# Performance work log

Measured on AMD Instinct MI355X. Metric: run time of the kernel, lower is better.

Reference implementation:

```python
import jax, jax.numpy as jnp
import numpy as np

B, BS, M, D = 64, 8, 512, 256  # b = bs * neg_sample_num, neg_sample_num = 8
NEG_FILL = -1e10


def setup_inputs() -> dict:
    key = jax.random.key(0)
    ks = jax.random.split(key, 7)
    x = jax.random.normal(ks[0], (B, M, D), jnp.float32)
    y = jax.random.normal(ks[1], (BS, M, D), jnp.float32)
    mask_x = jax.random.randint(ks[2], (B, M), 0, 2).astype(bool).at[:, 0].set(True)
    mask_y = jax.random.randint(ks[3], (BS, M), 0, 2).astype(bool).at[:, 0].set(True)
    scale = 1.0 / np.sqrt(D)
    Wq = jax.random.normal(ks[4], (D, D), jnp.float32) * scale  # torch Linear weight [out,in]
    Wk = jax.random.normal(ks[5], (D, D), jnp.float32) * scale
    Wv = jax.random.normal(ks[6], (D, D), jnp.float32) * scale
    return {"x": x, "y": y, "mask_x": mask_x, "mask_y": mask_y, "Wq": Wq, "Wk": Wk, "Wv": Wv}


def reference(x, y, mask_x, mask_y, Wq, Wk, Wv):
    # Projections (torch Linear: x @ W.T, no bias)
    Qx, Kx, Vx = x @ Wq.T, x @ Wk.T, x @ Wv.T
    Qy, Ky, Vy = y @ Wq.T, y @ Wk.T, y @ Wv.T
    b, m, d = Qx.shape
    bs = Ky.shape[0]
    neg = b // bs  # neg_sample_num branch (bs != b)

    scores_x = jnp.einsum('bid,bjd->bij', Qx, Kx)   # [b,m,m]
    scores_y = jnp.einsum('bid,bjd->bij', Qy, Ky)   # [bs,m,m]
    # Q_x grouped as [bs, neg, m, d] then transposed to [neg, bs, m, d];
    # K_y is tiled over neg (pure broadcast), so contract directly against [bs,m,d].
    Qx_e = Qx.reshape(bs, neg, m, d).swapaxes(0, 1)  # [neg,bs,m,d]
    scores_xy = jnp.einsum('nsid,sjd->nsij', Qx_e, Ky)  # [neg,bs,m,m]

    mx = mask_x[:, :, None]  # [b,m,1]
    my = mask_y[:, :, None]  # [bs,m,1]
    scores_x = jnp.where(mx & mx.swapaxes(1, 2), scores_x, NEG_FILL)
    scores_y = jnp.where(my & my.swapaxes(1, 2), scores_y, NEG_FILL)

    mask_xy = mask_x.reshape(bs, neg, m, 1).swapaxes(0, 1) & mask_y[None, :, None, :]  # [neg,bs,m,m]
    scores_xy = jnp.where(mask_xy, scores_xy, NEG_FILL)

    # y_len[n, s] = sum(mask_y[s]) for every n (repeat/view/sum/transpose in torch)
    y_len = jnp.broadcast_to(jnp.sum(mask_y.astype(jnp.int32), axis=1)[None, :], (neg, bs))

    probs_x = jax.nn.softmax(scores_x, axis=-1)
    probs_y = jax.nn.softmax(scores_y, axis=-1)
    probs_xy = jax.nn.softmax(scores_xy, axis=-1)

    ctx_x = jnp.einsum('bij,bjd->bid', probs_x, Vx)
    ctx_y = jnp.einsum('bij,bjd->bid', probs_y, Vy)
    return (ctx_x, ctx_y, scores_x, scores_y, probs_xy, mask_xy, y_len)
```

## Files before the change

kernel.cpp:

```cpp
#include <hip/hip_runtime.h>
#include <cstdint>

#define NEG_FILL_F (-10000000000.0f)
constexpr int BB     = 64;
constexpr int BS_    = 8;
constexpr int MM     = 512;
constexpr int DD     = 256;
constexpr int ROWS_X = BB * MM;
constexpr int ROWS_Y = BS_ * MM;
constexpr int ROWS_ALL = ROWS_X + ROWS_Y;
constexpr int K3     = 768;

typedef __attribute__((ext_vector_type(8))) short short8;
typedef __attribute__((ext_vector_type(4))) float f32x4;

__device__ inline unsigned short rne_bf16(float f) {
    unsigned int u = __float_as_uint(f);
    u = (u + 0x7FFFu + ((u >> 16) & 1u)) >> 16;
    return (unsigned short)u;
}
__device__ inline float bf2f(unsigned short h) {
    return __uint_as_float(((unsigned int)h) << 16);
}

__device__ inline f32x4 mfma16(short8 a, short8 b, f32x4 c) {
    return __builtin_amdgcn_mfma_f32_16x16x32_bf16(a, b, c, 0, 0, 0);
}

__device__ inline void gld16(const unsigned short* g, unsigned short* l) {
    __builtin_amdgcn_global_load_lds(
        (const __attribute__((address_space(1))) unsigned int*)g,
        (__attribute__((address_space(3))) unsigned int*)l, 16, 0, 0);
}

template<int LDA, int LDB>
__device__ inline void mfma_tiles(const unsigned short (*Ab)[LDA],
                                  const unsigned short (*Bb)[LDB],
                                  int kk, int wrow, int wcol, int lid, int quad,
                                  f32x4 acc[4][4])
{
    short8 af[4], bfr[4];
    #pragma unroll
    for (int i = 0; i < 4; ++i)
        af[i] = *(const short8*)&Ab[wrow + i * 16 + lid][kk + quad * 8];
    #pragma unroll
    for (int j = 0; j < 4; ++j)
        bfr[j] = *(const short8*)&Bb[wcol + j * 16 + lid][kk + quad * 8];
    #pragma unroll
    for (int i = 0; i < 4; ++i)
        #pragma unroll
        for (int j = 0; j < 4; ++j)
            acc[i][j] = mfma16(af[i], bfr[j], acc[i][j]);
}

__device__ inline void stage768_async(unsigned short* dstbase,
                                      const unsigned short* __restrict__ src,
                                      int ck, int wave, int lane)
{
    #pragma unroll
    for (int s = 0; s < 6; ++s) {
        const int c   = s * 256 + wave * 64 + lane;
        const int row = c / 12;
        const int kc  = (c % 12) * 8;
        gld16(src + (size_t)row * K3 + ck * 96 + kc,
              dstbase + (size_t)(s * 256 + wave * 64) * 8);
    }
}

__device__ inline void stage_x96(unsigned short (*dst)[96],
                                 const float* __restrict__ src,
                                 int ck, int t)
{
    #pragma unroll
    for (int s = 0; s < 4; ++s) {
        const int c   = s * 256 + t;
        const int row = c >> 3;
        const int q4  = (c & 7) * 4;
        float4 v = *(const float4*)(src + (size_t)row * DD + ck * 32 + q4);
        const float fv[4] = {v.x, v.y, v.z, v.w};
        unsigned short o[12];
        #pragma unroll
        for (int e = 0; e < 4; ++e) {
            unsigned short h = rne_bf16(fv[e]);
            unsigned short l = rne_bf16(fv[e] - bf2f(h));
            o[e*3+0] = h; o[e*3+1] = l; o[e*3+2] = h;
        }
        ushort4* p = (ushort4*)&dst[row][q4 * 3];
        p[0] = make_ushort4(o[0], o[1], o[2],  o[3]);
        p[1] = make_ushort4(o[4], o[5], o[6],  o[7]);
        p[2] = make_ushort4(o[8], o[9], o[10], o[11]);
    }
}

__global__ __launch_bounds__(256) void convw_kernel(
    const float* __restrict__ Wq, const float* __restrict__ Wk,
    const float* __restrict__ Wv, unsigned short* __restrict__ Wb)
{
    const int g  = blockIdx.x * 256 + threadIdx.x;
    const int e  = g * 8;
    const int zi = e >> 16;
    const int off = e & 65535;
    const float* W = (zi == 0) ? Wq : (zi == 1 ? Wk : Wv);
    float4 v0 = *(const float4*)(W + off);
    float4 v1 = *(const float4*)(W + off + 4);
    const float fv[8] = {v0.x, v0.y, v0.z, v0.w, v1.x, v1.y, v1.z, v1.w};
    unsigned short o[24];
    #pragma unroll
    for (int i = 0; i < 8; ++i) {
        unsigned short h = rne_bf16(fv[i]);
        unsigned short l = rne_bf16(fv[i] - bf2f(h));
        o[i*3+0] = h; o[i*3+1] = h; o[i*3+2] = l;
    }
    unsigned short* dst = Wb + (size_t)zi * 196608 + (size_t)off * 3;
    #pragma unroll
    for (int s = 0; s < 3; ++s) {
        short8 v;
        #pragma unroll
        for (int e2 = 0; e2 < 8; ++e2) v[e2] = (short)o[s*8+e2];
        *(short8*)(dst + s * 8) = v;
    }
}

__global__ __launch_bounds__(256) void proj_kernel(
    const float* __restrict__ x, const float* __restrict__ y,
    const unsigned short* __restrict__ Wb,
    unsigned short* __restrict__ Qa, unsigned short* __restrict__ Kb,
    unsigned short* __restrict__ Vt)
{
    const int z    = blockIdx.z;
    const int row0 = blockIdx.x * 128;
    const int col0 = blockIdx.y * 128;
    const float* A = (row0 < ROWS_X) ? (x + (size_t)row0 * DD)
                                     : (y + (size_t)(row0 - ROWS_X) * DD);
    const unsigned short* Bsrc = Wb + (size_t)z * 196608 + (size_t)col0 * K3;

    __shared__ unsigned short Ab[128][96];
    __shared__ unsigned short Bb[128][96];

    const int t = threadIdx.x;
    const int wave = t >> 6, lane = t & 63, quad = lane >> 4, lid = lane & 15;
    const int wrow = (wave & 1) * 64, wcol = (wave >> 1) * 64;

    f32x4 acc[4][4];
    #pragma unroll
    for (int i = 0; i < 4; ++i)
        #pragma unroll
        for (int j = 0; j < 4; ++j) acc[i][j] = (f32x4){0.f, 0.f, 0.f, 0.f};

    for (int ck = 0; ck < 8; ++ck) {
        stage768_async(&Bb[0][0], Bsrc, ck, wave, lane);
        stage_x96(Ab, A, ck, t);
        __syncthreads();
        #pragma unroll
        for (int kk = 0; kk < 96; kk += 32)
            mfma_tiles<96,96>(Ab, Bb, kk, wrow, wcol, lid, quad, acc);
        __syncthreads();
    }

    if (z == 2) {
        #pragma unroll
        for (int i = 0; i < 4; ++i) {
            const int rg = row0 + wrow + i * 16 + quad * 4;
            const int b  = rg >> 9;
            const int j  = rg & 511;
            #pragma unroll
            for (int jt = 0; jt < 4; ++jt) {
                const int col = col0 + wcol + jt * 16 + lid;
                *(ushort4*)(Vt + (size_t)b * DD * MM + (size_t)col * MM + j) =
                    make_ushort4(rne_bf16(acc[i][jt][0]), rne_bf16(acc[i][jt][1]),
                                 rne_bf16(acc[i][jt][2]), rne_bf16(acc[i][jt][3]));
            }
        }
    } else {
        unsigned short* dst = (z == 0) ? Qa : Kb;
        const bool aform = (z == 0);
        #pragma unroll
        for (int i = 0; i < 4; ++i) {
            const int rg = row0 + wrow + i * 16 + quad * 4;
            #pragma unroll
            for (int r = 0; r < 4; ++r) {
                unsigned short* rowp = dst + (size_t)(rg + r) * K3;
                #pragma unroll
                for (int jt = 0; jt < 4; ++jt) {
                    const int col = col0 + wcol + jt * 16 + lid;
                    const float v = acc[i][jt][r];
                    unsigned short h = rne_bf16(v);
                    unsigned short l = rne_bf16(v - bf2f(h));
                    rowp[3*col+0] = h;
                    rowp[3*col+1] = aform ? l : h;
                    rowp[3*col+2] = aform ? h : l;
                }
            }
        }
    }
}

__global__ __launch_bounds__(256) void scores_kernel(
    const unsigned short* __restrict__ Qa_base,
    const unsigned short* __restrict__ Kb_base,
    const int* __restrict__ mq_base, const int* __restrict__ mk_base,
    float* __restrict__ Sbase, float* __restrict__ Mbase,
    float2* __restrict__ pstats, int mode)
{
    const int z = blockIdx.z;
    int bq, bk;
    if (mode == 2) { const int n = z >> 3, s = z & 7; bq = s * 8 + n; bk = s; }
    else           { bq = z; bk = z; }

    const int row0 = blockIdx.x * 128;
    const int col0 = blockIdx.y * 128;
    const unsigned short* Asrc = Qa_base + (size_t)(bq * MM + row0) * K3;
    const unsigned short* Bsrc = Kb_base + (size_t)(bk * MM + col0) * K3;
    const int* mq = mq_base + bq * MM;
    const int* mk = mk_base + bk * MM;
    float* S  = Sbase + (size_t)z * MM * MM;
    float* Mo = (mode == 2) ? (Mbase + (size_t)z * MM * MM) : nullptr;

    __shared__ unsigned short Ab[128][96];
    __shared__ unsigned short Bb[128][96];
    __shared__ float pm2[128][2];
    __shared__ float ps2[128][2];

    const int t = threadIdx.x;
    const int wave = t >> 6, lane = t & 63, quad = lane >> 4, lid = lane & 15;
    const int wrow = (wave & 1) * 64, wcol = (wave >> 1) * 64;

    f32x4 acc[4][4];
    #pragma unroll
    for (int i = 0; i < 4; ++i)
        #pragma unroll
        for (int j = 0; j < 4; ++j) acc[i][j] = (f32x4){0.f, 0.f, 0.f, 0.f};

    for (int ck = 0; ck < 8; ++ck) {
        stage768_async(&Ab[0][0], Asrc, ck, wave, lane);
        stage768_async(&Bb[0][0], Bsrc, ck, wave, lane);
        __syncthreads();
        #pragma unroll
        for (int kk = 0; kk < 96; kk += 32)
            mfma_tiles<96,96>(Ab, Bb, kk, wrow, wcol, lid, quad, acc);
        __syncthreads();
    }

    int mcol[4];
    #pragma unroll
    for (int jt = 0; jt < 4; ++jt) mcol[jt] = mk[col0 + wcol + jt * 16 + lid];

    #pragma unroll
    for (int i = 0; i < 4; ++i) {
        const int rl0 = wrow + i * 16 + quad * 4;
        #pragma unroll
        for (int r = 0; r < 4; ++r) {
            const int rlocal = rl0 + r;
            const int rg = row0 + rlocal;
            const bool mr = (mq[rg] != 0);
            float* Srow = S + (size_t)rg * MM;
            float* Mrow = Mo ? (Mo + (size_t)rg * MM) : nullptr;
            float v[4];
            float mt = -3.4e38f;
            #pragma unroll
            for (int jt = 0; jt < 4; ++jt) {
                const int col = col0 + wcol + jt * 16 + lid;
                const bool valid = mr && (mcol[jt] != 0);
                v[jt] = valid ? acc[i][jt][r] : NEG_FILL_F;
                Srow[col] = v[jt];
                if (Mrow) Mrow[col] = valid ? 1.0f : 0.0f;
                mt = fmaxf(mt, v[jt]);
            }
            #pragma unroll
            for (int o = 1; o < 16; o <<= 1) mt = fmaxf(mt, __shfl_xor(mt, o));
            float se = 0.f;
            #pragma unroll
            for (int jt = 0; jt < 4; ++jt) se += __expf(v[jt] - mt);
            #pragma unroll
            for (int o = 1; o < 16; o <<= 1) se += __shfl_xor(se, o);
            if (lid == 0) { pm2[rlocal][wave >> 1] = mt; ps2[rlocal][wave >> 1] = se; }
        }
    }
    __syncthreads();
    if (t < 128) {
        const float m0 = pm2[t][0], m1 = pm2[t][1];
        const float mm = fmaxf(m0, m1);
        const float ss = ps2[t][0] * __expf(m0 - mm) + ps2[t][1] * __expf(m1 - mm);
        pstats[(size_t)(z * 4 + blockIdx.y) * MM + row0 + t] = make_float2(mm, ss);
    }
}

__global__ __launch_bounds__(256) void reduce4_kernel(
    const float2* __restrict__ p, float2* __restrict__ st)
{
    const int row = blockIdx.x * 256 + threadIdx.x;
    const int z = row >> 9, rl = row & 511;
    float m = -3.4e38f, s = 0.f;
    #pragma unroll
    for (int by = 0; by < 4; ++by) {
        float2 v = p[(size_t)(z * 4 + by) * MM + rl];
        float nm = fmaxf(m, v.x);
        s = s * __expf(m - nm) + v.y * __expf(v.x - nm);
        m = nm;
    }
    st[row] = make_float2(m, 1.0f / s);
}

__global__ __launch_bounds__(256) void ctx_kernel(
    const float* __restrict__ Sbase, const float2* __restrict__ stats,
    const unsigned short* __restrict__ Vt_base, float* __restrict__ Obase)
{
    const int b = blockIdx.z;
    const float*          S  = Sbase + (size_t)b * MM * MM;
    const float2*         st = stats + (size_t)b * MM;
    const unsigned short* Vt = Vt_base + (size_t)b * DD * MM;
    float*                O  = Obase + (size_t)b * MM * DD;

    const int row0 = blockIdx.x * 128;
    const int col0 = blockIdx.y * 128;

    __shared__ unsigned short Ab[128][72];
    __shared__ unsigned short Bb[128][64];

    const int t = threadIdx.x;
    const int wave = t >> 6, lane = t & 63, quad = lane >> 4, lid = lane & 15;
    const int wrow = (wave & 1) * 64, wcol = (wave >> 1) * 64;

    f32x4 acc[4][4];
    #pragma unroll
    for (int i = 0; i < 4; ++i)
        #pragma unroll
        for (int j = 0; j < 4; ++j) acc[i][j] = (f32x4){0.f, 0.f, 0.f, 0.f};

    for (int ck = 0; ck < 8; ++ck) {
        #pragma unroll
        for (int s = 0; s < 4; ++s) {
            const int c   = s * 256 + wave * 64 + lane;
            const int row = c >> 3;
            const int j8  = (c & 7) * 8;
            gld16(Vt + (size_t)(col0 + row) * MM + ck * 64 + j8,
                  &Bb[0][0] + (size_t)(s * 256 + wave * 64) * 8);
        }
        #pragma unroll
        for (int s = 0; s < 4; ++s) {
            const int c   = s * 256 + t;
            const int row = c >> 3;
            const int j8  = (c & 7) * 8;
            const float* sp = S + (size_t)(row0 + row) * MM + ck * 64 + j8;
            float4 v0 = *(const float4*)sp;
            float4 v1 = *(const float4*)(sp + 4);
            const float pm = st[row0 + row].x;
            short8 pk;
            pk[0] = (short)rne_bf16(__expf(v0.x - pm));
            pk[1] = (short)rne_bf16(__expf(v0.y - pm));
            pk[2] = (short)rne_bf16(__expf(v0.z - pm));
            pk[3] = (short)rne_bf16(__expf(v0.w - pm));
            pk[4] = (short)rne_bf16(__expf(v1.x - pm));
            pk[5] = (short)rne_bf16(__expf(v1.y - pm));
            pk[6] = (short)rne_bf16(__expf(v1.z - pm));
            pk[7] = (short)rne_bf16(__expf(v1.w - pm));
            *(short8*)&Ab[row][j8] = pk;
        }
        __syncthreads();
        #pragma unroll
        for (int kk = 0; kk < 64; kk += 32)
            mfma_tiles<72,64>(Ab, Bb, kk, wrow, wcol, lid, quad, acc);
        __syncthreads();
    }

    #pragma unroll
    for (int i = 0; i < 4; ++i) {
        const int rgb = row0 + wrow + i * 16 + quad * 4;
        float inv[4];
        #pragma unroll
        for (int r = 0; r < 4; ++r) inv[r] = st[rgb + r].y;
        #pragma unroll
        for (int jt = 0; jt < 4; ++jt) {
            const int col = col0 + wcol + jt * 16 + lid;
            #pragma unroll
            for (int r = 0; r < 4; ++r)
                O[(size_t)(rgb + r) * DD + col] = acc[i][jt][r] * inv[r];
        }
    }
}

__global__ __launch_bounds__(128) void softmax_apply(
    float* __restrict__ S, const float2* __restrict__ stats)
{
    const int row = blockIdx.x;
    const float2 st = stats[row];
    float4* r = (float4*)(S + (size_t)row * MM) + threadIdx.x;
    float4 v = *r;
    v.x = __expf(v.x - st.x) * st.y;
    v.y = __expf(v.y - st.x) * st.y;
    v.z = __expf(v.z - st.x) * st.y;
    v.w = __expf(v.w - st.x) * st.y;
    *r = v;
}

__global__ void ylen_kernel(const int* __restrict__ mask_y, float* __restrict__ out)
{
    const int s = blockIdx.x;
    const int lane = threadIdx.x;
    int c = 0;
    #pragma unroll
    for (int k = 0; k < 8; ++k) c += (mask_y[s * MM + k * 64 + lane] != 0);
    #pragma unroll
    for (int off = 32; off; off >>= 1) c += __shfl_xor(c, off);
    if (lane < 8) out[lane * 8 + s] = (float)c;
}

extern "C" void kernel_launch(void* const* d_in, const int* in_sizes, int n_in,
                              void* d_out, int out_size, void* d_ws, size_t ws_size,
                              hipStream_t stream)
{
    const float* x      = (const float*)d_in[0];
    const float* y      = (const float*)d_in[1];
    const int*   mask_x = (const int*)d_in[2];
    const int*   mask_y = (const int*)d_in[3];
    const float* Wq     = (const float*)d_in[4];
    const float* Wk     = (const float*)d_in[5];
    const float* Wv     = (const float*)d_in[6];
    float* out = (float*)d_out;

    unsigned short* Wb = (unsigned short*)d_ws;
    unsigned short* Qa = Wb + 589824;
    unsigned short* Kb = Qa + 28311552;
    unsigned short* Vt = Kb + 28311552;
    float2* stats_x  = (float2*)(Vt + 9437184);
    float2* stats_y  = stats_x + ROWS_X;
    float2* stats_xy = stats_y + ROWS_Y;
    float2* ps_x  = stats_xy + ROWS_X;
    float2* ps_y  = ps_x + 64 * 4 * 512;
    float2* ps_xy = ps_y + 8 * 4 * 512;

    float* out_ctx_x = out;
    float* out_ctx_y = out + 8388608;
    float* out_sx    = out + 9437184;
    float* out_sy    = out + 26214400;
    float* out_pxy   = out + 28311552;
    float* out_mxy   = out + 45088768;
    float* out_ylen  = out + 61865984;

    convw_kernel<<<96, 256, 0, stream>>>(Wq, Wk, Wv, Wb);

    proj_kernel<<<dim3(288, 2, 3), 256, 0, stream>>>(x, y, Wb, Qa, Kb, Vt);

    const unsigned short* Qa_y = Qa + (size_t)ROWS_X * K3;
    const unsigned short* Kb_y = Kb + (size_t)ROWS_X * K3;

    scores_kernel<<<dim3(4, 4, 64), 256, 0, stream>>>(Qa,   Kb,   mask_x, mask_x, out_sx,  nullptr, ps_x,  0);
    scores_kernel<<<dim3(4, 4, 8),  256, 0, stream>>>(Qa_y, Kb_y, mask_y, mask_y, out_sy,  nullptr, ps_y,  1);
    scores_kernel<<<dim3(4, 4, 64), 256, 0, stream>>>(Qa,   Kb_y, mask_x, mask_y, out_pxy, out_mxy, ps_xy, 2);

    reduce4_kernel<<<ROWS_X / 256, 256, 0, stream>>>(ps_x,  stats_x);
    reduce4_kernel<<<ROWS_Y / 256, 256, 0, stream>>>(ps_y,  stats_y);
    reduce4_kernel<<<ROWS_X / 256, 256, 0, stream>>>(ps_xy, stats_xy);

    ctx_kernel<<<dim3(4, 2, 64), 256, 0, stream>>>(out_sx, stats_x, Vt, out_ctx_x);
    ctx_kernel<<<dim3(4, 2, 8),  256, 0, stream>>>(out_sy, stats_y,
                                                   Vt + (size_t)64 * DD * MM, out_ctx_y);

    softmax_apply<<<ROWS_X, 128, 0, stream>>>(out_pxy, stats_xy);

    ylen_kernel<<<8, 64, 0, stream>>>(mask_y, out_ylen);
}
```

Baseline: 550.4 us.

## Split bf16x3 operands into separate hi/lo planes and stage epilogues via LDS

Replaces the interleaved 768-wide bf16x3 operand format with separate hi and lo bf16 arrays of width 256. A conversion kernel pre-splits x, y and the weights, so proj no longer converts activations inline. The GEMM loops become 12 chunks of 64 using the same three-product split. Proj epilogues now go through swizzled LDS for coalesced 16-byte stores, including the transposed V. The mask_xy output moves out of the scores kernel into its own kernel, and the ctx kernel hoists its row-max loads. This adds an extra pass over x/y and more barriers per GEMM, but cuts the byte-granular scattered stores.

```diff
diff --git a/kernel.cpp b/kernel.cpp
--- a/kernel.cpp
+++ b/kernel.cpp
@@ -9,7 +9,6 @@
 constexpr int ROWS_X = BB * MM;
 constexpr int ROWS_Y = BS_ * MM;
 constexpr int ROWS_ALL = ROWS_X + ROWS_Y;
-constexpr int K3     = 768;
 
 typedef __attribute__((ext_vector_type(8))) short short8;
 typedef __attribute__((ext_vector_type(4))) float f32x4;
@@ -22,11 +21,9 @@
 __device__ inline float bf2f(unsigned short h) {
     return __uint_as_float(((unsigned int)h) << 16);
 }
-
 __device__ inline f32x4 mfma16(short8 a, short8 b, f32x4 c) {
     return __builtin_amdgcn_mfma_f32_16x16x32_bf16(a, b, c, 0, 0, 0);
 }
-
 __device__ inline void gld16(const unsigned short* g, unsigned short* l) {
     __builtin_amdgcn_global_load_lds(
         (const __attribute__((address_space(1))) unsigned int*)g,
@@ -53,89 +50,68 @@
             acc[i][j] = mfma16(af[i], bfr[j], acc[i][j]);
 }
 
-__device__ inline void stage768_async(unsigned short* dstbase,
-                                      const unsigned short* __restrict__ src,
-                                      int ck, int wave, int lane)
-{
-    #pragma unroll
-    for (int s = 0; s < 6; ++s) {
+__device__ inline void stage64_async(unsigned short* dstbase,
+                                     const unsigned short* __restrict__ src,
+                                     int wave, int lane)
+{
+    #pragma unroll
+    for (int s = 0; s < 4; ++s) {
         const int c   = s * 256 + wave * 64 + lane;
-        const int row = c / 12;
-        const int kc  = (c % 12) * 8;
-        gld16(src + (size_t)row * K3 + ck * 96 + kc,
+        const int row = c >> 3;
+        const int off = (c & 7) * 8;
+        gld16(src + (size_t)row * 256 + off,
               dstbase + (size_t)(s * 256 + wave * 64) * 8);
     }
 }
 
-__device__ inline void stage_x96(unsigned short (*dst)[96],
-                                 const float* __restrict__ src,
-                                 int ck, int t)
-{
-    #pragma unroll
-    for (int s = 0; s < 4; ++s) {
-        const int c   = s * 256 + t;
-        const int row = c >> 3;
-        const int q4  = (c & 7) * 4;
-        float4 v = *(const float4*)(src + (size_t)row * DD + ck * 32 + q4);
-        const float fv[4] = {v.x, v.y, v.z, v.w};
-        unsigned short o[12];
-        #pragma unroll
-        for (int e = 0; e < 4; ++e) {
-            unsigned short h = rne_bf16(fv[e]);
-            unsigned short l = rne_bf16(fv[e] - bf2f(h));
-            o[e*3+0] = h; o[e*3+1] = l; o[e*3+2] = h;
-        }
-        ushort4* p = (ushort4*)&dst[row][q4 * 3];
-        p[0] = make_ushort4(o[0], o[1], o[2],  o[3]);
-        p[1] = make_ushort4(o[4], o[5], o[6],  o[7]);
-        p[2] = make_ushort4(o[8], o[9], o[10], o[11]);
-    }
-}
-
-__global__ __launch_bounds__(256) void convw_kernel(
+__global__ __launch_bounds__(256) void conv_kernel(
+    const float* __restrict__ x, const float* __restrict__ y,
     const float* __restrict__ Wq, const float* __restrict__ Wk,
-    const float* __restrict__ Wv, unsigned short* __restrict__ Wb)
-{
-    const int g  = blockIdx.x * 256 + threadIdx.x;
-    const int e  = g * 8;
-    const int zi = e >> 16;
-    const int off = e & 65535;
-    const float* W = (zi == 0) ? Wq : (zi == 1 ? Wk : Wv);
-    float4 v0 = *(const float4*)(W + off);
-    float4 v1 = *(const float4*)(W + off + 4);
+    const float* __restrict__ Wv,
+    unsigned short* __restrict__ Xh, unsigned short* __restrict__ Xl,
+    unsigned short* __restrict__ Wh, unsigned short* __restrict__ Wl)
+{
+    const size_t e = ((size_t)blockIdx.x * 256 + threadIdx.x) * 8;
+    const float* src; unsigned short *dh, *dl;
+    if (e < 9437184) {
+        src = (e < 8388608) ? (x + e) : (y + (e - 8388608));
+        dh = Xh + e; dl = Xl + e;
+    } else {
+        const size_t ew = e - 9437184;
+        const int zi = (int)(ew >> 16);
+        src = (zi == 0 ? Wq : zi == 1 ? Wk : Wv) + (ew & 65535);
+        dh = Wh + ew; dl = Wl + ew;
+    }
+    float4 v0 = *(const float4*)src;
+    float4 v1 = *(const float4*)(src + 4);
     const float fv[8] = {v0.x, v0.y, v0.z, v0.w, v1.x, v1.y, v1.z, v1.w};
-    unsigned short o[24];
+    short8 h8, l8;
     #pragma unroll
     for (int i = 0; i < 8; ++i) {
         unsigned short h = rne_bf16(fv[i]);
-        unsigned short l = rne_bf16(fv[i] - bf2f(h));
-        o[i*3+0] = h; o[i*3+1] = h; o[i*3+2] = l;
-    }
-    unsigned short* dst = Wb + (size_t)zi * 196608 + (size_t)off * 3;
-    #pragma unroll
-    for (int s = 0; s < 3; ++s) {
-        short8 v;
-        #pragma unroll
-        for (int e2 = 0; e2 < 8; ++e2) v[e2] = (short)o[s*8+e2];
-        *(short8*)(dst + s * 8) = v;
-    }
+        h8[i] = (short)h;
+        l8[i] = (short)rne_bf16(fv[i] - bf2f(h));
+    }
+    *(short8*)dh = h8;
+    *(short8*)dl = l8;
 }
 
 __global__ __launch_bounds__(256) void proj_kernel(
-    const float* __restrict__ x, const float* __restrict__ y,
-    const unsigned short* __restrict__ Wb,
-    unsigned short* __restrict__ Qa, unsigned short* __restrict__ Kb,
+    const unsigned short* __restrict__ Xh, const unsigned short* __restrict__ Xl,
+    const unsigned short* __restrict__ Wh, const unsigned short* __restrict__ Wl,
+    unsigned short* __restrict__ Qh, unsigned short* __restrict__ Ql,
+    unsigned short* __restrict__ Kh, unsigned short* __restrict__ Kl,
     unsigned short* __restrict__ Vt)
 {
     const int z    = blockIdx.z;
     const int row0 = blockIdx.x * 128;
     const int col0 = blockIdx.y * 128;
-    const float* A = (row0 < ROWS_X) ? (x + (size_t)row0 * DD)
-                                     : (y + (size_t)(row0 - ROWS_X) * DD);
-    const unsigned short* Bsrc = Wb + (size_t)z * 196608 + (size_t)col0 * K3;
-
-    __shared__ unsigned short Ab[128][96];
-    __shared__ unsigned short Bb[128][96];
+    const unsigned short* WhP = Wh + (size_t)z * 65536;
+    const unsigned short* WlP = Wl + (size_t)z * 65536;
+
+    __shared__ unsigned short POOL[16384];
+    unsigned short (*Ab)[64] = (unsigned short (*)[64])POOL;
+    unsigned short (*Bb)[64] = (unsigned short (*)[64])(POOL + 8192);
 
     const int t = threadIdx.x;
     const int wave = t >> 6, lane = t & 63, quad = lane >> 4, lid = lane & 15;
@@ -147,60 +123,86 @@
         #pragma unroll
         for (int j = 0; j < 4; ++j) acc[i][j] = (f32x4){0.f, 0.f, 0.f, 0.f};
 
-    for (int ck = 0; ck < 8; ++ck) {
-        stage768_async(&Bb[0][0], Bsrc, ck, wave, lane);
-        stage_x96(Ab, A, ck, t);
-        __syncthreads();
-        #pragma unroll
-        for (int kk = 0; kk < 96; kk += 32)
-            mfma_tiles<96,96>(Ab, Bb, kk, wrow, wcol, lid, quad, acc);
+    for (int ck = 0; ck < 12; ++ck) {
+        const int s  = ck >> 2;
+        const int d0 = (ck & 3) * 64;
+        const unsigned short* Ap = (s == 2 ? Xl : Xh) + (size_t)row0 * 256 + d0;
+        const unsigned short* Bp = (s == 1 ? WlP : WhP) + (size_t)col0 * 256 + d0;
+        stage64_async(&Ab[0][0], Ap, wave, lane);
+        stage64_async(&Bb[0][0], Bp, wave, lane);
+        __syncthreads();
+        mfma_tiles<64,64>(Ab, Bb, 0,  wrow, wcol, lid, quad, acc);
+        mfma_tiles<64,64>(Ab, Bb, 32, wrow, wcol, lid, quad, acc);
         __syncthreads();
     }
 
     if (z == 2) {
         #pragma unroll
         for (int i = 0; i < 4; ++i) {
-            const int rg = row0 + wrow + i * 16 + quad * 4;
-            const int b  = rg >> 9;
-            const int j  = rg & 511;
+            const int tok0 = wrow + i * 16 + quad * 4;
             #pragma unroll
             for (int jt = 0; jt < 4; ++jt) {
-                const int col = col0 + wcol + jt * 16 + lid;
-                *(ushort4*)(Vt + (size_t)b * DD * MM + (size_t)col * MM + j) =
-                    make_ushort4(rne_bf16(acc[i][jt][0]), rne_bf16(acc[i][jt][1]),
-                                 rne_bf16(acc[i][jt][2]), rne_bf16(acc[i][jt][3]));
+                const int d  = wcol + jt * 16 + lid;
+                const int sw = ((d >> 2) & 7) << 4;
+                unsigned int lo = (unsigned)rne_bf16(acc[i][jt][0]) |
+                                  ((unsigned)rne_bf16(acc[i][jt][1]) << 16);
+                unsigned int hi = (unsigned)rne_bf16(acc[i][jt][2]) |
+                                  ((unsigned)rne_bf16(acc[i][jt][3]) << 16);
+                *(uint2*)&POOL[d * 128 + (tok0 ^ sw)] = make_uint2(lo, hi);
             }
         }
+        __syncthreads();
+        const int dloc = t >> 1, cb = (t & 1) * 64;
+        const int sw = ((dloc >> 2) & 7) << 4;
+        const int b = row0 >> 9, j0 = row0 & 511;
+        unsigned short* gdst = Vt + ((size_t)b * DD + col0 + dloc) * MM + j0 + cb;
+        #pragma unroll
+        for (int g = 0; g < 8; ++g) {
+            short8 v = *(const short8*)&POOL[dloc * 128 + ((cb + g * 8) ^ sw)];
+            *(short8*)(gdst + g * 8) = v;
+        }
     } else {
-        unsigned short* dst = (z == 0) ? Qa : Kb;
-        const bool aform = (z == 0);
-        #pragma unroll
-        for (int i = 0; i < 4; ++i) {
-            const int rg = row0 + wrow + i * 16 + quad * 4;
-            #pragma unroll
-            for (int r = 0; r < 4; ++r) {
-                unsigned short* rowp = dst + (size_t)(rg + r) * K3;
+        unsigned short* dstH = (z == 0) ? Qh : Kh;
+        unsigned short* dstL = (z == 0) ? Ql : Kl;
+        #pragma unroll
+        for (int p = 0; p < 2; ++p) {
+            #pragma unroll
+            for (int i = 0; i < 4; ++i) {
+                const int rl = wrow + i * 16 + quad * 4;
                 #pragma unroll
-                for (int jt = 0; jt < 4; ++jt) {
-                    const int col = col0 + wcol + jt * 16 + lid;
-                    const float v = acc[i][jt][r];
-                    unsigned short h = rne_bf16(v);
-                    unsigned short l = rne_bf16(v - bf2f(h));
-                    rowp[3*col+0] = h;
-                    rowp[3*col+1] = aform ? l : h;
-                    rowp[3*col+2] = aform ? h : l;
+                for (int r = 0; r < 4; ++r) {
+                    const int row = rl + r;
+                    const int sw  = ((row >> 2) & 7) << 4;
+                    #pragma unroll
+                    for (int jt = 0; jt < 4; ++jt) {
+                        const int col = wcol + jt * 16 + lid;
+                        const float v = acc[i][jt][r];
+                        const unsigned short h = rne_bf16(v);
+                        POOL[row * 128 + (col ^ sw)] =
+                            (p == 0) ? h : rne_bf16(v - bf2f(h));
+                    }
                 }
             }
+            __syncthreads();
+            const int rr = t >> 1, cb = (t & 1) * 64;
+            const int sw = ((rr >> 2) & 7) << 4;
+            unsigned short* gdst = (p == 0 ? dstH : dstL)
+                                 + (size_t)(row0 + rr) * 256 + col0 + cb;
+            #pragma unroll
+            for (int g = 0; g < 8; ++g) {
+                short8 v = *(const short8*)&POOL[rr * 128 + ((cb + g * 8) ^ sw)];
+                *(short8*)(gdst + g * 8) = v;
+            }
+            __syncthreads();
         }
     }
 }
 
 __global__ __launch_bounds__(256) void scores_kernel(
-    const unsigned short* __restrict__ Qa_base,
-    const unsigned short* __restrict__ Kb_base,
+    const unsigned short* __restrict__ Qh_, const unsigned short* __restrict__ Ql_,
+    const unsigned short* __restrict__ Kh_, const unsigned short* __restrict__ Kl_,
     const int* __restrict__ mq_base, const int* __restrict__ mk_base,
-    float* __restrict__ Sbase, float* __restrict__ Mbase,
-    float2* __restrict__ pstats, int mode)
+    float* __restrict__ Sbase, float2* __restrict__ pstats, int mode)
 {
     const int z = blockIdx.z;
     int bq, bk;
@@ -209,15 +211,15 @@
 
     const int row0 = blockIdx.x * 128;
     const int col0 = blockIdx.y * 128;
-    const unsigned short* Asrc = Qa_base + (size_t)(bq * MM + row0) * K3;
-    const unsigned short* Bsrc = Kb_base + (size_t)(bk * MM + col0) * K3;
+    const size_t aoff = (size_t)(bq * MM + row0) * 256;
+    const size_t boff = (size_t)(bk * MM + col0) * 256;
     const int* mq = mq_base + bq * MM;
     const int* mk = mk_base + bk * MM;
-    float* S  = Sbase + (size_t)z * MM * MM;
-    float* Mo = (mode == 2) ? (Mbase + (size_t)z * MM * MM) : nullptr;
-
-    __shared__ unsigned short Ab[128][96];
-    __shared__ unsigned short Bb[128][96];
+    float* S = Sbase + (size_t)z * MM * MM;
+
+    __shared__ unsigned short POOL[16384];
+    unsigned short (*Ab)[64] = (unsigned short (*)[64])POOL;
+    unsigned short (*Bb)[64] = (unsigned short (*)[64])(POOL + 8192);
     __shared__ float pm2[128][2];
     __shared__ float ps2[128][2];
 
@@ -231,13 +233,16 @@
         #pragma unroll
         for (int j = 0; j < 4; ++j) acc[i][j] = (f32x4){0.f, 0.f, 0.f, 0.f};
 
-    for (int ck = 0; ck < 8; ++ck) {
-        stage768_async(&Ab[0][0], Asrc, ck, wave, lane);
-        stage768_async(&Bb[0][0], Bsrc, ck, wave, lane);
-        __syncthreads();
-        #pragma unroll
-        for (int kk = 0; kk < 96; kk += 32)
-            mfma_tiles<96,96>(Ab, Bb, kk, wrow, wcol, lid, quad, acc);
+    for (int ck = 0; ck < 12; ++ck) {
+        const int s  = ck >> 2;
+        const int d0 = (ck & 3) * 64;
+        const unsigned short* Ap = (s == 2 ? Ql_ : Qh_) + aoff + d0;
+        const unsigned short* Bp = (s == 1 ? Kl_ : Kh_) + boff + d0;
+        stage64_async(&Ab[0][0], Ap, wave, lane);
+        stage64_async(&Bb[0][0], Bp, wave, lane);
+        __syncthreads();
+        mfma_tiles<64,64>(Ab, Bb, 0,  wrow, wcol, lid, quad, acc);
+        mfma_tiles<64,64>(Ab, Bb, 32, wrow, wcol, lid, quad, acc);
         __syncthreads();
     }
 
@@ -254,7 +259,6 @@
             const int rg = row0 + rlocal;
             const bool mr = (mq[rg] != 0);
             float* Srow = S + (size_t)rg * MM;
-            float* Mrow = Mo ? (Mo + (size_t)rg * MM) : nullptr;
             float v[4];
             float mt = -3.4e38f;
             #pragma unroll
@@ -263,7 +267,6 @@
                 const bool valid = mr && (mcol[jt] != 0);
                 v[jt] = valid ? acc[i][jt][r] : NEG_FILL_F;
                 Srow[col] = v[jt];
-                if (Mrow) Mrow[col] = valid ? 1.0f : 0.0f;
                 mt = fmaxf(mt, v[jt]);
             }
             #pragma unroll
@@ -285,6 +288,28 @@
     }
 }
 
+__global__ __launch_bounds__(256) void maskxy_kernel(
+    const int* __restrict__ mask_x, const int* __restrict__ mask_y,
+    float* __restrict__ Mo)
+{
+    const int z = blockIdx.y;
+    const int n = z >> 3, s = z & 7, bq = s * 8 + n;
+    const int i = blockIdx.x * 4 + (threadIdx.x >> 6);
+    const int lane = threadIdx.x & 63;
+    const bool mr = mask_x[bq * MM + i] != 0;
+    float* row = Mo + ((size_t)z * MM + i) * MM;
+    const int4* my = (const int4*)(mask_y + s * MM);
+    #pragma unroll
+    for (int g = 0; g < 2; ++g) {
+        const int c4 = g * 64 + lane;
+        int4 m4 = my[c4];
+        float4 v = mr ? make_float4(m4.x ? 1.f : 0.f, m4.y ? 1.f : 0.f,
+                                    m4.z ? 1.f : 0.f, m4.w ? 1.f : 0.f)
+                      : make_float4(0.f, 0.f, 0.f, 0.f);
+        *(float4*)(row + c4 * 4) = v;
+    }
+}
+
 __global__ __launch_bounds__(256) void reduce4_kernel(
     const float2* __restrict__ p, float2* __restrict__ st)
 {
@@ -326,6 +351,10 @@
     for (int i = 0; i < 4; ++i)
         #pragma unroll
         for (int j = 0; j < 4; ++j) acc[i][j] = (f32x4){0.f, 0.f, 0.f, 0.f};
+
+    float pmv[4];
+    #pragma unroll
+    for (int s = 0; s < 4; ++s) pmv[s] = st[row0 + ((s * 256 + t) >> 3)].x;
 
     for (int ck = 0; ck < 8; ++ck) {
         #pragma unroll
@@ -344,7 +373,7 @@
             const float* sp = S + (size_t)(row0 + row) * MM + ck * 64 + j8;
             float4 v0 = *(const float4*)sp;
             float4 v1 = *(const float4*)(sp + 4);
-            const float pm = st[row0 + row].x;
+            const float pm = pmv[s];
             short8 pk;
             pk[0] = (short)rne_bf16(__expf(v0.x - pm));
             pk[1] = (short)rne_bf16(__expf(v0.y - pm));
@@ -357,9 +386,8 @@
             *(short8*)&Ab[row][j8] = pk;
         }
         __syncthreads();
-        #pragma unroll
-        for (int kk = 0; kk < 64; kk += 32)
-            mfma_tiles<72,64>(Ab, Bb, kk, wrow, wcol, lid, quad, acc);
+        mfma_tiles<72,64>(Ab, Bb, 0,  wrow, wcol, lid, quad, acc);
+        mfma_tiles<72,64>(Ab, Bb, 32, wrow, wcol, lid, quad, acc);
         __syncthreads();
     }
 
@@ -418,10 +446,15 @@
     const float* Wv     = (const float*)d_in[6];
     float* out = (float*)d_out;
 
-    unsigned short* Wb = (unsigned short*)d_ws;
-    unsigned short* Qa = Wb + 589824;
-    unsigned short* Kb = Qa + 28311552;
-    unsigned short* Vt = Kb + 28311552;
+    unsigned short* Xh = (unsigned short*)d_ws;
+    unsigned short* Xl = Xh + 9437184;
+    unsigned short* Wh = Xl + 9437184;
+    unsigned short* Wl = Wh + 196608;
+    unsigned short* Qh = Wl + 196608;
+    unsigned short* Ql = Qh + 9437184;
+    unsigned short* Kh = Ql + 9437184;
+    unsigned short* Kl = Kh + 9437184;
+    unsigned short* Vt = Kl + 9437184;
     float2* stats_x  = (float2*)(Vt + 9437184);
     float2* stats_y  = stats_x + ROWS_X;
     float2* stats_xy = stats_y + ROWS_Y;
@@ -437,16 +470,24 @@
     float* out_mxy   = out + 45088768;
     float* out_ylen  = out + 61865984;
 
-    convw_kernel<<<96, 256, 0, stream>>>(Wq, Wk, Wv, Wb);
-
-    proj_kernel<<<dim3(288, 2, 3), 256, 0, stream>>>(x, y, Wb, Qa, Kb, Vt);
-
-    const unsigned short* Qa_y = Qa + (size_t)ROWS_X * K3;
-    const unsigned short* Kb_y = Kb + (size_t)ROWS_X * K3;
-
-    scores_kernel<<<dim3(4, 4, 64), 256, 0, stream>>>(Qa,   Kb,   mask_x, mask_x, out_sx,  nullptr, ps_x,  0);
-    scores_kernel<<<dim3(4, 4, 8),  256, 0, stream>>>(Qa_y, Kb_y, mask_y, mask_y, out_sy,  nullptr, ps_y,  1);
-    scores_kernel<<<dim3(4, 4, 64), 256, 0, stream>>>(Qa,   Kb_y, mask_x, mask_y, out_pxy, out_mxy, ps_xy, 2);
+    conv_kernel<<<4704, 256, 0, stream>>>(x, y, Wq, Wk, Wv, Xh, Xl, Wh, Wl);
+
+    proj_kernel<<<dim3(288, 2, 3), 256, 0, stream>>>(Xh, Xl, Wh, Wl,
+                                                     Qh, Ql, Kh, Kl, Vt);
+
+    const unsigned short* Qh_y = Qh + (size_t)ROWS_X * 256;
+    const unsigned short* Ql_y = Ql + (size_t)ROWS_X * 256;
+    const unsigned short* Kh_y = Kh + (size_t)ROWS_X * 256;
+    const unsigned short* Kl_y = Kl + (size_t)ROWS_X * 256;
+
+    scores_kernel<<<dim3(4, 4, 64), 256, 0, stream>>>(Qh,   Ql,   Kh,   Kl,
+        mask_x, mask_x, out_sx, ps_x, 0);
+    scores_kernel<<<dim3(4, 4, 8),  256, 0, stream>>>(Qh_y, Ql_y, Kh_y, Kl_y,
+        mask_y, mask_y, out_sy, ps_y, 1);
+    scores_kernel<<<dim3(4, 4, 64), 256, 0, stream>>>(Qh,   Ql,   Kh_y, Kl_y,
+        mask_x, mask_y, out_pxy, ps_xy, 2);
+
+    maskxy_kernel<<<dim3(128, 64), 256, 0, stream>>>(mask_x, mask_y, out_mxy);
 
     reduce4_kernel<<<ROWS_X / 256, 256, 0, stream>>>(ps_x,  stats_x);
     reduce4_kernel<<<ROWS_Y / 256, 256, 0, stream>>>(ps_y,  stats_y);
```

Result: slower. 630.9 us (+14.6%).
